# Optimization experiments

Hardware: AMD Instinct MI355X
Metric: run time of the kernel (lower is better)

The kernel has to match this reference:

```python
import jax, jax.numpy as jnp
import numpy as np

DT = 0.03125                                   # ray-march step size
NSTEPS = int(np.ceil(2.0 * np.sqrt(3.0) / DT)) # enough steps to cross the [-1,1]^3 cube diagonal (=111)


def trilinear_sample(vol, pos):
    """vol: [C, D, Hv, Wv]; pos: [H, W, 3] xyz in [-1,1] (grid_sample convention,
    align_corners=True). Returns [C, H, W]."""
    D, Hv, Wv = vol.shape[1], vol.shape[2], vol.shape[3]

    def axis(g, n):
        g = jnp.clip((g + 1.0) * 0.5 * (n - 1), 0.0, n - 1.0)
        i0 = jnp.minimum(jnp.floor(g).astype(jnp.int32), n - 2)
        return i0, i0 + 1, (g - i0)[None]  # frac broadcast over channel dim

    x0, x1, fx = axis(pos[..., 0], Wv)
    y0, y1, fy = axis(pos[..., 1], Hv)
    z0, z1, fz = axis(pos[..., 2], D)

    def g(z, y, x):
        return vol[:, z, y, x]  # [C, H, W]

    c00 = g(z0, y0, x0) * (1 - fx) + g(z0, y0, x1) * fx
    c01 = g(z0, y1, x0) * (1 - fx) + g(z0, y1, x1) * fx
    c10 = g(z1, y0, x0) * (1 - fx) + g(z1, y0, x1) * fx
    c11 = g(z1, y1, x0) * (1 - fx) + g(z1, y1, x1) * fx
    c0 = c00 * (1 - fy) + c01 * fy
    c1 = c10 * (1 - fy) + c11 * fy
    return c0 * (1 - fz) + c1 * fz


def setup_inputs() -> dict:
    key = jax.random.key(0)
    B, H, W, D = 2, 256, 256, 128
    camrot = jnp.tile(jnp.eye(3, dtype=jnp.float32)[None], (B, 1, 1))
    campos = jnp.tile(jnp.array([[0.0, 0.0, -2.5]], dtype=jnp.float32), (B, 1))
    focal = jnp.full((B, 2), 300.0, dtype=jnp.float32)
    princpt = jnp.full((B, 2), 128.0, dtype=jnp.float32)
    ys, xs = jnp.meshgrid(jnp.arange(H, dtype=jnp.float32),
                          jnp.arange(W, dtype=jnp.float32), indexing='ij')
    pixelcoords = jnp.tile(jnp.stack([xs, ys], axis=-1)[None], (B, 1, 1, 1))
    volume = jax.random.uniform(key, (B, 4, D, D, D), dtype=jnp.float32)
    return dict(camrot=camrot, campos=campos, focal=focal, princpt=princpt,
                pixelcoords=pixelcoords, volume=volume)


def reference(camrot, campos, focal, princpt, pixelcoords, volume):
    # camera rays: pixel -> camera -> world (camrot^T applied, as in torch sum over dim=-2)
    raydir = (pixelcoords - princpt[:, None, None, :]) / focal[:, None, None, :]
    raydir = jnp.concatenate([raydir, jnp.ones_like(raydir[..., :1])], axis=-1)
    raydir = jnp.einsum('bij,bhwi->bhwj', camrot, raydir)
    raydir = raydir / jnp.sqrt(jnp.sum(raydir ** 2, axis=-1, keepdims=True))

    # ray-AABB intersection with [-1,1]^3 (no grad, as in torch.no_grad())
    t1 = (-1.0 - campos[:, None, None, :]) / raydir
    t2 = (1.0 - campos[:, None, None, :]) / raydir
    tmin = jnp.maximum(jnp.minimum(t1[..., 0], t2[..., 0]),
                       jnp.maximum(jnp.minimum(t1[..., 1], t2[..., 1]),
                                   jnp.minimum(t1[..., 2], t2[..., 2])))
    tmax = jnp.minimum(jnp.maximum(t1[..., 0], t2[..., 0]),
                       jnp.minimum(jnp.maximum(t1[..., 1], t2[..., 1]),
                                   jnp.maximum(t1[..., 2], t2[..., 2])))
    hit = tmin < tmax
    t0 = jax.lax.stop_gradient(jnp.maximum(jnp.where(hit, tmin, 0.0), 0.0))

    raypos = campos[:, None, None, :] + raydir * t0[..., None]  # [B,H,W,3]
    B, H, W = raypos.shape[:3]
    rayrgb = jnp.zeros((B, 3, H, W), raypos.dtype)
    rayalpha = jnp.zeros((B, 1, H, W), raypos.dtype)

    def step(carry, _):
        raypos, rayrgb, rayalpha = carry
        valid = jnp.all((raypos > -1.0) & (raypos < 1.0), axis=-1).astype(raypos.dtype)
        samp = jax.vmap(trilinear_sample)(volume, raypos)  # [B,4,H,W]
        contrib = (jnp.minimum(rayalpha + samp[:, 3:4] * DT, 1.0) - rayalpha) * valid[:, None]
        rayrgb = rayrgb + samp[:, :3] * contrib
        rayalpha = rayalpha + contrib
        raypos = raypos + raydir * DT
        return (raypos, rayrgb, rayalpha), None

    (_, rayrgb, rayalpha), _ = jax.lax.scan(step, (raypos, rayrgb, rayalpha),
                                            None, length=NSTEPS)
    return jnp.concatenate([rayrgb, rayalpha], axis=1)  # [B,4,H,W]
```

## Files before the change

kernel.cpp:

```cpp
#include <hip/hip_runtime.h>
#include <math.h>

#pragma clang fp contract(off)

#define DT 0.03125f
#define NSTEPS 111

__device__ __forceinline__ float4 lerp4(float4 a, float4 b, float w) {
#pragma clang fp contract(off)
    float wa = 1.0f - w;
    float4 r;
    r.x = a.x * wa + b.x * w;
    r.y = a.y * wa + b.y * w;
    r.z = a.z * wa + b.z * w;
    r.w = a.w * wa + b.w * w;
    return r;
}

__global__ __launch_bounds__(256) void repack_kernel(const float* __restrict__ vol,
                                                     float4* __restrict__ out,
                                                     long total, long spatial) {
    long idx = (long)blockIdx.x * blockDim.x + threadIdx.x;
    if (idx >= total) return;
    long b = idx / spatial;
    long s = idx - b * spatial;
    const float* p = vol + b * 4 * spatial + s;
    float4 v;
    v.x = p[0];
    v.y = p[spatial];
    v.z = p[2 * spatial];
    v.w = p[3 * spatial];
    out[idx] = v;
}

template <bool PACKED>
__global__ __launch_bounds__(256) void raymarch_kernel(
        const float* __restrict__ camrot, const float* __restrict__ campos,
        const float* __restrict__ focal, const float* __restrict__ princpt,
        const float* __restrict__ pixelcoords, const float* __restrict__ vol,
        float* __restrict__ out, int B, int H, int W, int D) {
#pragma clang fp contract(off)
    int x = blockIdx.x * blockDim.x + threadIdx.x;
    int y = blockIdx.y * blockDim.y + threadIdx.y;
    int b = blockIdx.z;
    if (x >= W || y >= H) return;

    long pidx = (((long)b * H + y) * W + x) * 2;
    float px = pixelcoords[pidx];
    float py = pixelcoords[pidx + 1];
    const float* R = camrot + b * 9;
    float cpx = campos[b * 3 + 0], cpy = campos[b * 3 + 1], cpz = campos[b * 3 + 2];
    float flx = focal[b * 2 + 0], fly = focal[b * 2 + 1];
    float prx = princpt[b * 2 + 0], pry = princpt[b * 2 + 1];

    float rx = (px - prx) / flx;
    float ry = (py - pry) / fly;
    float rz = 1.0f;
    float dx = R[0] * rx + R[3] * ry + R[6] * rz;
    float dy = R[1] * rx + R[4] * ry + R[7] * rz;
    float dz = R[2] * rx + R[5] * ry + R[8] * rz;
    float ss = dx * dx;
    ss = ss + dy * dy;
    ss = ss + dz * dz;
    float nrm = sqrtf(ss);
    dx = dx / nrm; dy = dy / nrm; dz = dz / nrm;

    float t1x = (-1.0f - cpx) / dx, t2x = (1.0f - cpx) / dx;
    float t1y = (-1.0f - cpy) / dy, t2y = (1.0f - cpy) / dy;
    float t1z = (-1.0f - cpz) / dz, t2z = (1.0f - cpz) / dz;
    float tmin = fmaxf(fminf(t1x, t2x), fmaxf(fminf(t1y, t2y), fminf(t1z, t2z)));
    float tmax = fminf(fmaxf(t1x, t2x), fminf(fmaxf(t1y, t2y), fmaxf(t1z, t2z)));
    bool hit = tmin < tmax;
    float t0 = fmaxf(hit ? tmin : 0.0f, 0.0f);

    float posx = cpx + dx * t0;
    float posy = cpy + dy * t0;
    float posz = cpz + dz * t0;
    float stx = dx * DT, sty = dy * DT, stz = dz * DT;

    float accr = 0.0f, accg = 0.0f, accb = 0.0f, alpha = 0.0f;
    float gmax = (float)(D - 1);
    long spatial = (long)D * D * D;
    long zstride = (long)D * D;
    const float4* v4 = reinterpret_cast<const float4*>(vol);
    const float* vb = vol + (long)b * 4 * spatial;
    long b4base = (long)b * spatial;

    bool entered = false;
    for (int s = 0; s < NSTEPS; ++s) {
        bool valid = (posx > -1.0f) && (posx < 1.0f) &&
                     (posy > -1.0f) && (posy < 1.0f) &&
                     (posz > -1.0f) && (posz < 1.0f);
        if (valid) {
            entered = true;
            float gx = fminf(fmaxf((posx + 1.0f) * 0.5f * gmax, 0.0f), gmax);
            float gy = fminf(fmaxf((posy + 1.0f) * 0.5f * gmax, 0.0f), gmax);
            float gz = fminf(fmaxf((posz + 1.0f) * 0.5f * gmax, 0.0f), gmax);
            int ix0 = (int)floorf(gx); if (ix0 > D - 2) ix0 = D - 2;
            int iy0 = (int)floorf(gy); if (iy0 > D - 2) iy0 = D - 2;
            int iz0 = (int)floorf(gz); if (iz0 > D - 2) iz0 = D - 2;
            float fx = gx - (float)ix0;
            float fy = gy - (float)iy0;
            float fz = gz - (float)iz0;

            float4 c000, c001, c010, c011, c100, c101, c110, c111;
            if (PACKED) {
                long base = b4base + (long)iz0 * zstride + (long)iy0 * D + ix0;
                c000 = v4[base];
                c001 = v4[base + 1];
                c010 = v4[base + D];
                c011 = v4[base + D + 1];
                c100 = v4[base + zstride];
                c101 = v4[base + zstride + 1];
                c110 = v4[base + zstride + D];
                c111 = v4[base + zstride + D + 1];
            } else {
                long s000 = (long)iz0 * zstride + (long)iy0 * D + ix0;
                #define FETCH(dst, off) { long o_ = (off); \
                    dst.x = vb[o_]; dst.y = vb[o_ + spatial]; \
                    dst.z = vb[o_ + 2 * spatial]; dst.w = vb[o_ + 3 * spatial]; }
                FETCH(c000, s000);
                FETCH(c001, s000 + 1);
                FETCH(c010, s000 + D);
                FETCH(c011, s000 + D + 1);
                FETCH(c100, s000 + zstride);
                FETCH(c101, s000 + zstride + 1);
                FETCH(c110, s000 + zstride + D);
                FETCH(c111, s000 + zstride + D + 1);
                #undef FETCH
            }
            float4 c00 = lerp4(c000, c001, fx);
            float4 c01 = lerp4(c010, c011, fx);
            float4 c10 = lerp4(c100, c101, fx);
            float4 c11 = lerp4(c110, c111, fx);
            float4 c0 = lerp4(c00, c01, fy);
            float4 c1 = lerp4(c10, c11, fy);
            float4 samp = lerp4(c0, c1, fz);

            float contrib = fminf(alpha + samp.w * DT, 1.0f) - alpha;
            accr = accr + samp.x * contrib;
            accg = accg + samp.y * contrib;
            accb = accb + samp.z * contrib;
            alpha = alpha + contrib;
            if (alpha >= 1.0f) break;
        } else if (entered) {
            break;
        }
        posx = posx + stx; posy = posy + sty; posz = posz + stz;
    }

    long hw = (long)H * W;
    long o = (long)b * 4 * hw + (long)y * W + x;
    out[o] = accr;
    out[o + hw] = accg;
    out[o + 2 * hw] = accb;
    out[o + 3 * hw] = alpha;
}

extern "C" void kernel_launch(void* const* d_in, const int* in_sizes, int n_in,
                              void* d_out, int out_size, void* d_ws, size_t ws_size,
                              hipStream_t stream) {
    const float* camrot = (const float*)d_in[0];
    const float* campos = (const float*)d_in[1];
    const float* focal = (const float*)d_in[2];
    const float* princpt = (const float*)d_in[3];
    const float* pixelcoords = (const float*)d_in[4];
    const float* volume = (const float*)d_in[5];
    float* out = (float*)d_out;

    int B = in_sizes[0] / 9;
    long spatial = (long)in_sizes[5] / (B * 4);
    int D = (int)lround(cbrt((double)spatial));
    while ((long)D * D * D > spatial) D--;
    while ((long)(D + 1) * (D + 1) * (D + 1) <= spatial) D++;
    long hw = (long)in_sizes[4] / (B * 2);
    int H = (int)lround(sqrt((double)hw));
    int W = H;

    size_t need = (size_t)B * spatial * 4 * sizeof(float);
    dim3 blk(16, 16, 1);
    dim3 grd((W + 15) / 16, (H + 15) / 16, B);

    if (ws_size >= need) {
        long total = (long)B * spatial;
        int th = 256;
        long nb = (total + th - 1) / th;
        repack_kernel<<<dim3((unsigned)nb), dim3(th), 0, stream>>>(volume, (float4*)d_ws,
                                                                   total, spatial);
        raymarch_kernel<true><<<grd, blk, 0, stream>>>(camrot, campos, focal, princpt,
                                                       pixelcoords, (const float*)d_ws,
                                                       out, B, H, W, D);
    } else {
        raymarch_kernel<false><<<grd, blk, 0, stream>>>(camrot, campos, focal, princpt,
                                                        pixelcoords, volume,
                                                        out, B, H, W, D);
    }
}
```

Baseline: 164.8 us.

## Software-pipeline voxel gathers in raymarch and vectorize volume repack

Replaces the raymarch loop with a two-stage software pipeline. A pre-pass first counts the valid in-cube steps and finds the entry point, then the loads for the next sample are issued while the current one is blended. The early termination on alpha saturation is removed. The repack kernel is vectorized to read float4 quads from each channel and transpose them into interleaved RGBA. This targets gather latency and repack bandwidth, at the cost of higher register use and an extra ALU pre-pass.

```diff
diff --git a/kernel.cpp b/kernel.cpp
--- a/kernel.cpp
+++ b/kernel.cpp
@@ -15,6 +15,26 @@
     r.z = a.z * wa + b.z * w;
     r.w = a.w * wa + b.w * w;
     return r;
+}
+
+
+__global__ __launch_bounds__(256) void repack4_kernel(const float* __restrict__ vol,
+                                                      float4* __restrict__ out,
+                                                      long spatial) {
+    long q = (long)blockIdx.x * blockDim.x + threadIdx.x;
+    long nq = spatial >> 2;
+    if (q >= nq) return;
+    long b = blockIdx.y;
+    const float* p = vol + b * 4 * spatial + (q << 2);
+    float4 c0 = *(const float4*)(p);
+    float4 c1 = *(const float4*)(p + spatial);
+    float4 c2 = *(const float4*)(p + 2 * spatial);
+    float4 c3 = *(const float4*)(p + 3 * spatial);
+    float4* o = out + b * spatial + (q << 2);
+    o[0] = make_float4(c0.x, c1.x, c2.x, c3.x);
+    o[1] = make_float4(c0.y, c1.y, c2.y, c3.y);
+    o[2] = make_float4(c0.z, c1.z, c2.z, c3.z);
+    o[3] = make_float4(c0.w, c1.w, c2.w, c3.w);
 }
 
 __global__ __launch_bounds__(256) void repack_kernel(const float* __restrict__ vol,
@@ -33,11 +53,57 @@
     out[idx] = v;
 }
 
-template <bool PACKED>
-__global__ __launch_bounds__(256) void raymarch_kernel(
+
+__device__ __forceinline__ int voxel_base(float posx, float posy, float posz,
+                                          int D, float gmax, int zstride,
+                                          float& fx, float& fy, float& fz) {
+#pragma clang fp contract(off)
+    float gx = fminf(fmaxf((posx + 1.0f) * 0.5f * gmax, 0.0f), gmax);
+    float gy = fminf(fmaxf((posy + 1.0f) * 0.5f * gmax, 0.0f), gmax);
+    float gz = fminf(fmaxf((posz + 1.0f) * 0.5f * gmax, 0.0f), gmax);
+    int ix0 = (int)floorf(gx); if (ix0 > D - 2) ix0 = D - 2;
+    int iy0 = (int)floorf(gy); if (iy0 > D - 2) iy0 = D - 2;
+    int iz0 = (int)floorf(gz); if (iz0 > D - 2) iz0 = D - 2;
+    fx = gx - (float)ix0;
+    fy = gy - (float)iy0;
+    fz = gz - (float)iz0;
+    return iz0 * zstride + iy0 * D + ix0;
+}
+
+__device__ __forceinline__ void load8(const float4* __restrict__ v4, int base,
+                                      int D, int zstride, float4* c) {
+    c[0] = v4[base];
+    c[1] = v4[base + 1];
+    c[2] = v4[base + D];
+    c[3] = v4[base + D + 1];
+    c[4] = v4[base + zstride];
+    c[5] = v4[base + zstride + 1];
+    c[6] = v4[base + zstride + D];
+    c[7] = v4[base + zstride + D + 1];
+}
+
+__device__ __forceinline__ void accum_step(const float4* c, float fx, float fy, float fz,
+                                           float& accr, float& accg, float& accb,
+                                           float& alpha) {
+#pragma clang fp contract(off)
+    float4 c00 = lerp4(c[0], c[1], fx);
+    float4 c01 = lerp4(c[2], c[3], fx);
+    float4 c10 = lerp4(c[4], c[5], fx);
+    float4 c11 = lerp4(c[6], c[7], fx);
+    float4 c0 = lerp4(c00, c01, fy);
+    float4 c1 = lerp4(c10, c11, fy);
+    float4 samp = lerp4(c0, c1, fz);
+    float contrib = fminf(alpha + samp.w * DT, 1.0f) - alpha;
+    accr = accr + samp.x * contrib;
+    accg = accg + samp.y * contrib;
+    accb = accb + samp.z * contrib;
+    alpha = alpha + contrib;
+}
+
+__global__ __launch_bounds__(256, 1) void raymarch_pipe_kernel(
         const float* __restrict__ camrot, const float* __restrict__ campos,
         const float* __restrict__ focal, const float* __restrict__ princpt,
-        const float* __restrict__ pixelcoords, const float* __restrict__ vol,
+        const float* __restrict__ pixelcoords, const float4* __restrict__ vol4,
         float* __restrict__ out, int B, int H, int W, int D) {
 #pragma clang fp contract(off)
     int x = blockIdx.x * blockDim.x + threadIdx.x;
@@ -78,13 +144,119 @@
     float posz = cpz + dz * t0;
     float stx = dx * DT, sty = dy * DT, stz = dz * DT;
 
+    int n = 0;
+    float e0x = 0.0f, e0y = 0.0f, e0z = 0.0f;
+    {
+        float sx = posx, sy = posy, sz = posz;
+        int firstv = -1;
+        for (int s = 0; s < NSTEPS; ++s) {
+            bool valid = (sx > -1.0f) && (sx < 1.0f) &&
+                         (sy > -1.0f) && (sy < 1.0f) &&
+                         (sz > -1.0f) && (sz < 1.0f);
+            if (valid) {
+                if (firstv < 0) { firstv = s; e0x = sx; e0y = sy; e0z = sz; }
+                n++;
+            } else if (firstv >= 0) {
+                break;
+            }
+            sx = sx + stx; sy = sy + sty; sz = sz + stz;
+        }
+    }
+
+    float accr = 0.0f, accg = 0.0f, accb = 0.0f, alpha = 0.0f;
+    float gmax = (float)(D - 1);
+    int zstride = D * D;
+    int spatial = zstride * D;
+    const float4* v4b = vol4 + (long)b * spatial;
+
+    if (n > 0) {
+        float pxx = e0x, pyy = e0y, pzz = e0z;
+        float fxA, fyA, fzA, fxB = 0.f, fyB = 0.f, fzB = 0.f;
+        float4 A[8], Bv[8];
+
+        int baseA = voxel_base(pxx, pyy, pzz, D, gmax, zstride, fxA, fyA, fzA);
+        load8(v4b, baseA, D, zstride, A);
+        pxx = pxx + stx; pyy = pyy + sty; pzz = pzz + stz;
+
+        if (n > 1) {
+            int baseB = voxel_base(pxx, pyy, pzz, D, gmax, zstride, fxB, fyB, fzB);
+            load8(v4b, baseB, D, zstride, Bv);
+            pxx = pxx + stx; pyy = pyy + sty; pzz = pzz + stz;
+        }
+
+        int i = 0;
+        for (; i + 2 < n; i += 2) {
+            accum_step(A, fxA, fyA, fzA, accr, accg, accb, alpha);
+            int baseA2 = voxel_base(pxx, pyy, pzz, D, gmax, zstride, fxA, fyA, fzA);
+            load8(v4b, baseA2, D, zstride, A);
+            pxx = pxx + stx; pyy = pyy + sty; pzz = pzz + stz;
+
+            accum_step(Bv, fxB, fyB, fzB, accr, accg, accb, alpha);
+            int baseB2 = voxel_base(pxx, pyy, pzz, D, gmax, zstride, fxB, fyB, fzB);
+            load8(v4b, baseB2, D, zstride, Bv);
+            pxx = pxx + stx; pyy = pyy + sty; pzz = pzz + stz;
+        }
+        if (i < n) { accum_step(A, fxA, fyA, fzA, accr, accg, accb, alpha); i++; }
+        if (i < n) { accum_step(Bv, fxB, fyB, fzB, accr, accg, accb, alpha); }
+    }
+
+    long hw = (long)H * W;
+    long o = (long)b * 4 * hw + (long)y * W + x;
+    out[o] = accr;
+    out[o + hw] = accg;
+    out[o + 2 * hw] = accb;
+    out[o + 3 * hw] = alpha;
+}
+
+__global__ __launch_bounds__(256) void raymarch_simple_kernel(
+        const float* __restrict__ camrot, const float* __restrict__ campos,
+        const float* __restrict__ focal, const float* __restrict__ princpt,
+        const float* __restrict__ pixelcoords, const float* __restrict__ vol,
+        float* __restrict__ out, int B, int H, int W, int D) {
+#pragma clang fp contract(off)
+    int x = blockIdx.x * blockDim.x + threadIdx.x;
+    int y = blockIdx.y * blockDim.y + threadIdx.y;
+    int b = blockIdx.z;
+    if (x >= W || y >= H) return;
+
+    long pidx = (((long)b * H + y) * W + x) * 2;
+    float px = pixelcoords[pidx];
+    float py = pixelcoords[pidx + 1];
+    const float* R = camrot + b * 9;
+    float cpx = campos[b * 3 + 0], cpy = campos[b * 3 + 1], cpz = campos[b * 3 + 2];
+    float flx = focal[b * 2 + 0], fly = focal[b * 2 + 1];
+    float prx = princpt[b * 2 + 0], pry = princpt[b * 2 + 1];
+
+    float rx = (px - prx) / flx;
+    float ry = (py - pry) / fly;
+    float rz = 1.0f;
+    float dx = R[0] * rx + R[3] * ry + R[6] * rz;
+    float dy = R[1] * rx + R[4] * ry + R[7] * rz;
+    float dz = R[2] * rx + R[5] * ry + R[8] * rz;
+    float ss = dx * dx;
+    ss = ss + dy * dy;
+    ss = ss + dz * dz;
+    float nrm = sqrtf(ss);
+    dx = dx / nrm; dy = dy / nrm; dz = dz / nrm;
+
+    float t1x = (-1.0f - cpx) / dx, t2x = (1.0f - cpx) / dx;
+    float t1y = (-1.0f - cpy) / dy, t2y = (1.0f - cpy) / dy;
+    float t1z = (-1.0f - cpz) / dz, t2z = (1.0f - cpz) / dz;
+    float tmin = fmaxf(fminf(t1x, t2x), fmaxf(fminf(t1y, t2y), fminf(t1z, t2z)));
+    float tmax = fminf(fmaxf(t1x, t2x), fminf(fmaxf(t1y, t2y), fmaxf(t1z, t2z)));
+    bool hit = tmin < tmax;
+    float t0 = fmaxf(hit ? tmin : 0.0f, 0.0f);
+
+    float posx = cpx + dx * t0;
+    float posy = cpy + dy * t0;
+    float posz = cpz + dz * t0;
+    float stx = dx * DT, sty = dy * DT, stz = dz * DT;
+
     float accr = 0.0f, accg = 0.0f, accb = 0.0f, alpha = 0.0f;
     float gmax = (float)(D - 1);
     long spatial = (long)D * D * D;
     long zstride = (long)D * D;
-    const float4* v4 = reinterpret_cast<const float4*>(vol);
     const float* vb = vol + (long)b * 4 * spatial;
-    long b4base = (long)b * spatial;
 
     bool entered = false;
     for (int s = 0; s < NSTEPS; ++s) {
@@ -103,32 +275,20 @@
             float fy = gy - (float)iy0;
             float fz = gz - (float)iz0;
 
+            long s000 = (long)iz0 * zstride + (long)iy0 * D + ix0;
             float4 c000, c001, c010, c011, c100, c101, c110, c111;
-            if (PACKED) {
-                long base = b4base + (long)iz0 * zstride + (long)iy0 * D + ix0;
-                c000 = v4[base];
-                c001 = v4[base + 1];
-                c010 = v4[base + D];
-                c011 = v4[base + D + 1];
-                c100 = v4[base + zstride];
-                c101 = v4[base + zstride + 1];
-                c110 = v4[base + zstride + D];
-                c111 = v4[base + zstride + D + 1];
-            } else {
-                long s000 = (long)iz0 * zstride + (long)iy0 * D + ix0;
-                #define FETCH(dst, off) { long o_ = (off); \
-                    dst.x = vb[o_]; dst.y = vb[o_ + spatial]; \
-                    dst.z = vb[o_ + 2 * spatial]; dst.w = vb[o_ + 3 * spatial]; }
-                FETCH(c000, s000);
-                FETCH(c001, s000 + 1);
-                FETCH(c010, s000 + D);
-                FETCH(c011, s000 + D + 1);
-                FETCH(c100, s000 + zstride);
-                FETCH(c101, s000 + zstride + 1);
-                FETCH(c110, s000 + zstride + D);
-                FETCH(c111, s000 + zstride + D + 1);
-                #undef FETCH
-            }
+            #define FETCH(dst, off) { long o_ = (off); \
+                dst.x = vb[o_]; dst.y = vb[o_ + spatial]; \
+                dst.z = vb[o_ + 2 * spatial]; dst.w = vb[o_ + 3 * spatial]; }
+            FETCH(c000, s000);
+            FETCH(c001, s000 + 1);
+            FETCH(c010, s000 + D);
+            FETCH(c011, s000 + D + 1);
+            FETCH(c100, s000 + zstride);
+            FETCH(c101, s000 + zstride + 1);
+            FETCH(c110, s000 + zstride + D);
+            FETCH(c111, s000 + zstride + D + 1);
+            #undef FETCH
             float4 c00 = lerp4(c000, c001, fx);
             float4 c01 = lerp4(c010, c011, fx);
             float4 c10 = lerp4(c100, c101, fx);
@@ -182,16 +342,20 @@
     dim3 grd((W + 15) / 16, (H + 15) / 16, B);
 
     if (ws_size >= need) {
-        long total = (long)B * spatial;
-        int th = 256;
-        long nb = (total + th - 1) / th;
-        repack_kernel<<<dim3((unsigned)nb), dim3(th), 0, stream>>>(volume, (float4*)d_ws,
-                                                                   total, spatial);
-        raymarch_kernel<true><<<grd, blk, 0, stream>>>(camrot, campos, focal, princpt,
-                                                       pixelcoords, (const float*)d_ws,
-                                                       out, B, H, W, D);
+        if ((spatial & 3) == 0) {
+            long nq = spatial >> 2;
+            dim3 rgrd((unsigned)((nq + 255) / 256), B, 1);
+            repack4_kernel<<<rgrd, dim3(256), 0, stream>>>(volume, (float4*)d_ws, spatial);
+        } else {
+            long total = (long)B * spatial;
+            repack_kernel<<<dim3((unsigned)((total + 255) / 256)), dim3(256), 0, stream>>>(
+                volume, (float4*)d_ws, total, spatial);
+        }
+        raymarch_pipe_kernel<<<grd, blk, 0, stream>>>(camrot, campos, focal, princpt,
+                                                      pixelcoords, (const float4*)d_ws,
+                                                      out, B, H, W, D);
     } else {
-        raymarch_kernel<false><<<grd, blk, 0, stream>>>(camrot, campos, focal, princpt,
+        raymarch_simple_kernel<<<grd, blk, 0, stream>>>(camrot, campos, focal, princpt,
                                                         pixelcoords, volume,
                                                         out, B, H, W, D);
     }
```

Result: no change. 165.1 us (+0.1%).

## Split ray march into segments with sigma prefix pass and combine

Applied to the files above, without the earlier changes.

Each ray is split into four step segments run by separate threads. A first pass sums alpha increments per segment, and a second pass starts each segment from the clamped prefix alpha and accumulates colour. A combine kernel then adds the partial results. This aims to expose more parallelism and shorten each thread's serial loop, at the cost of a second volume traversal, extra launches, workspace traffic and dropping the early exit on saturated alpha. Starting a segment from the clamped prefix sum is only exact while alpha stays below one. The volume repack is also vectorised to float4 loads.

```diff
diff --git a/kernel.cpp b/kernel.cpp
--- a/kernel.cpp
+++ b/kernel.cpp
@@ -4,17 +4,29 @@
 #pragma clang fp contract(off)
 
 #define DT 0.03125f
+#define INV_DT 32.0f
 #define NSTEPS 111
-
-__device__ __forceinline__ float4 lerp4(float4 a, float4 b, float w) {
-#pragma clang fp contract(off)
-    float wa = 1.0f - w;
-    float4 r;
-    r.x = a.x * wa + b.x * w;
-    r.y = a.y * wa + b.y * w;
-    r.z = a.z * wa + b.z * w;
-    r.w = a.w * wa + b.w * w;
-    return r;
+#define SEG 4
+#define SLEN ((NSTEPS + SEG - 1) / SEG)
+
+
+__global__ __launch_bounds__(256) void repack4_kernel(const float* __restrict__ vol,
+                                                      float4* __restrict__ out,
+                                                      long spatial) {
+    long q = (long)blockIdx.x * blockDim.x + threadIdx.x;
+    long nq = spatial >> 2;
+    if (q >= nq) return;
+    long b = blockIdx.y;
+    const float* p = vol + b * 4 * spatial + (q << 2);
+    float4 c0 = *(const float4*)(p);
+    float4 c1 = *(const float4*)(p + spatial);
+    float4 c2 = *(const float4*)(p + 2 * spatial);
+    float4 c3 = *(const float4*)(p + 3 * spatial);
+    float4* o = out + b * spatial + (q << 2);
+    o[0] = make_float4(c0.x, c1.x, c2.x, c3.x);
+    o[1] = make_float4(c0.y, c1.y, c2.y, c3.y);
+    o[2] = make_float4(c0.z, c1.z, c2.z, c3.z);
+    o[3] = make_float4(c0.w, c1.w, c2.w, c3.w);
 }
 
 __global__ __launch_bounds__(256) void repack_kernel(const float* __restrict__ vol,
@@ -33,18 +45,20 @@
     out[idx] = v;
 }
 
-template <bool PACKED>
-__global__ __launch_bounds__(256) void raymarch_kernel(
-        const float* __restrict__ camrot, const float* __restrict__ campos,
-        const float* __restrict__ focal, const float* __restrict__ princpt,
-        const float* __restrict__ pixelcoords, const float* __restrict__ vol,
-        float* __restrict__ out, int B, int H, int W, int D) {
-#pragma clang fp contract(off)
-    int x = blockIdx.x * blockDim.x + threadIdx.x;
-    int y = blockIdx.y * blockDim.y + threadIdx.y;
-    int b = blockIdx.z;
-    if (x >= W || y >= H) return;
-
+
+struct Ray {
+    float posx, posy, posz;
+    float stx, sty, stz;
+    int n;
+};
+
+__device__ __forceinline__ Ray ray_setup(const float* __restrict__ camrot,
+                                         const float* __restrict__ campos,
+                                         const float* __restrict__ focal,
+                                         const float* __restrict__ princpt,
+                                         const float* __restrict__ pixelcoords,
+                                         int b, int y, int x, int H, int W) {
+#pragma clang fp contract(off)
     long pidx = (((long)b * H + y) * W + x) * 2;
     float px = pixelcoords[pidx];
     float py = pixelcoords[pidx + 1];
@@ -73,80 +87,264 @@
     bool hit = tmin < tmax;
     float t0 = fmaxf(hit ? tmin : 0.0f, 0.0f);
 
-    float posx = cpx + dx * t0;
-    float posy = cpy + dy * t0;
-    float posz = cpz + dz * t0;
-    float stx = dx * DT, sty = dy * DT, stz = dz * DT;
+    Ray r;
+    r.posx = cpx + dx * t0;
+    r.posy = cpy + dy * t0;
+    r.posz = cpz + dz * t0;
+    r.stx = dx * DT; r.sty = dy * DT; r.stz = dz * DT;
+
+    float span = (tmax - t0) * INV_DT + 4.0f;
+    span = fminf(span, (float)NSTEPS);
+    r.n = (hit && span > 0.0f) ? (int)span : 0;
+    return r;
+}
+
+__device__ __forceinline__ int voxel_base(float posx, float posy, float posz,
+                                          int D, float gmax, int zstride,
+                                          float& fx, float& fy, float& fz) {
+#pragma clang fp contract(off)
+    float gx = fminf(fmaxf((posx + 1.0f) * 0.5f * gmax, 0.0f), gmax);
+    float gy = fminf(fmaxf((posy + 1.0f) * 0.5f * gmax, 0.0f), gmax);
+    float gz = fminf(fmaxf((posz + 1.0f) * 0.5f * gmax, 0.0f), gmax);
+    int ix0 = (int)floorf(gx); if (ix0 > D - 2) ix0 = D - 2;
+    int iy0 = (int)floorf(gy); if (iy0 > D - 2) iy0 = D - 2;
+    int iz0 = (int)floorf(gz); if (iz0 > D - 2) iz0 = D - 2;
+    fx = gx - (float)ix0;
+    fy = gy - (float)iy0;
+    fz = gz - (float)iz0;
+    return iz0 * zstride + iy0 * D + ix0;
+}
+
+
+__global__ __launch_bounds__(256, 8) void sigma_pass_kernel(
+        const float* __restrict__ camrot, const float* __restrict__ campos,
+        const float* __restrict__ focal, const float* __restrict__ princpt,
+        const float* __restrict__ pixelcoords, const float4* __restrict__ vol4,
+        float* __restrict__ sums, int B, int H, int W, int D, int nrays) {
+#pragma clang fp contract(off)
+    int x = blockIdx.x * 16 + threadIdx.x;
+    int y = blockIdx.y * 16 + threadIdx.y;
+    int bz = blockIdx.z;
+    int b = bz / SEG;
+    int seg = bz - b * SEG;
+    if (x >= W || y >= H) return;
+    int ray = ((b * H + y) * W + x);
+
+    Ray r = ray_setup(camrot, campos, focal, princpt, pixelcoords, b, y, x, H, W);
+
+    int s0 = seg * SLEN;
+    int s1 = s0 + SLEN; if (s1 > NSTEPS) s1 = NSTEPS;
+    int lim = (r.n < s1) ? r.n : s1;
+
+    float S = 0.0f;
+    if (s0 < lim) {
+        float pxx = r.posx, pyy = r.posy, pzz = r.posz;
+        for (int s = 0; s < s0; ++s) {
+            pxx = pxx + r.stx; pyy = pyy + r.sty; pzz = pzz + r.stz;
+        }
+        float gmax = (float)(D - 1);
+        int zstride = D * D;
+        const float* vw = (const float*)(vol4 + (long)b * ((long)zstride * D));
+        for (int s = s0; s < lim; ++s) {
+            bool inside = (pxx > -1.0f) && (pxx < 1.0f) && (pyy > -1.0f) &&
+                          (pyy < 1.0f) && (pzz > -1.0f) && (pzz < 1.0f);
+            float m = inside ? 1.0f : 0.0f;
+            float fx, fy, fz;
+            int base = voxel_base(pxx, pyy, pzz, D, gmax, zstride, fx, fy, fz);
+            const float* p = vw + (long)base * 4 + 3;
+            float w000 = p[0],               w001 = p[4];
+            float w010 = p[4 * D],           w011 = p[4 * D + 4];
+            float w100 = p[4 * zstride],     w101 = p[4 * zstride + 4];
+            float w110 = p[4 * zstride + 4 * D], w111 = p[4 * zstride + 4 * D + 4];
+            float wa = 1.0f - fx;
+            float c00 = w000 * wa + w001 * fx;
+            float c01 = w010 * wa + w011 * fx;
+            float c10 = w100 * wa + w101 * fx;
+            float c11 = w110 * wa + w111 * fx;
+            float wb = 1.0f - fy;
+            float c0 = c00 * wb + c01 * fy;
+            float c1 = c10 * wb + c11 * fy;
+            float sw = c0 * (1.0f - fz) + c1 * fz;
+            S = S + (sw * DT) * m;
+            pxx = pxx + r.stx; pyy = pyy + r.sty; pzz = pzz + r.stz;
+        }
+    }
+    sums[(long)seg * nrays + ray] = S;
+}
+
+
+__global__ __launch_bounds__(256, 8) void march_pass_kernel(
+        const float* __restrict__ camrot, const float* __restrict__ campos,
+        const float* __restrict__ focal, const float* __restrict__ princpt,
+        const float* __restrict__ pixelcoords, const float4* __restrict__ vol4,
+        const float* __restrict__ sums, float* __restrict__ part,
+        int B, int H, int W, int D, int nrays) {
+#pragma clang fp contract(off)
+    int x = blockIdx.x * 16 + threadIdx.x;
+    int y = blockIdx.y * 16 + threadIdx.y;
+    int bz = blockIdx.z;
+    int b = bz / SEG;
+    int seg = bz - b * SEG;
+    if (x >= W || y >= H) return;
+    int ray = ((b * H + y) * W + x);
+
+    Ray r = ray_setup(camrot, campos, focal, princpt, pixelcoords, b, y, x, H, W);
+
+    float P = 0.0f;
+    for (int j = 0; j < seg; ++j) P = P + sums[(long)j * nrays + ray];
+    float alpha = fminf(P, 1.0f);
+
+    int s0 = seg * SLEN;
+    int s1 = s0 + SLEN; if (s1 > NSTEPS) s1 = NSTEPS;
+    int lim = (r.n < s1) ? r.n : s1;
+
+    float accr = 0.0f, accg = 0.0f, accb = 0.0f;
+    if (s0 < lim) {
+        float pxx = r.posx, pyy = r.posy, pzz = r.posz;
+        for (int s = 0; s < s0; ++s) {
+            pxx = pxx + r.stx; pyy = pyy + r.sty; pzz = pzz + r.stz;
+        }
+        float gmax = (float)(D - 1);
+        int zstride = D * D;
+        const float4* v4b = vol4 + (long)b * ((long)zstride * D);
+        for (int s = s0; s < lim; ++s) {
+            bool inside = (pxx > -1.0f) && (pxx < 1.0f) && (pyy > -1.0f) &&
+                          (pyy < 1.0f) && (pzz > -1.0f) && (pzz < 1.0f);
+            float m = inside ? 1.0f : 0.0f;
+            float fx, fy, fz;
+            int base = voxel_base(pxx, pyy, pzz, D, gmax, zstride, fx, fy, fz);
+            float4 c000 = v4b[base];
+            float4 c001 = v4b[base + 1];
+            float4 c010 = v4b[base + D];
+            float4 c011 = v4b[base + D + 1];
+            float4 c100 = v4b[base + zstride];
+            float4 c101 = v4b[base + zstride + 1];
+            float4 c110 = v4b[base + zstride + D];
+            float4 c111 = v4b[base + zstride + D + 1];
+            float wa = 1.0f - fx;
+            float4 c00, c01, c10, c11, c0, c1, samp;
+            c00.x = c000.x * wa + c001.x * fx; c00.y = c000.y * wa + c001.y * fx;
+            c00.z = c000.z * wa + c001.z * fx; c00.w = c000.w * wa + c001.w * fx;
+            c01.x = c010.x * wa + c011.x * fx; c01.y = c010.y * wa + c011.y * fx;
+            c01.z = c010.z * wa + c011.z * fx; c01.w = c010.w * wa + c011.w * fx;
+            c10.x = c100.x * wa + c101.x * fx; c10.y = c100.y * wa + c101.y * fx;
+            c10.z = c100.z * wa + c101.z * fx; c10.w = c100.w * wa + c101.w * fx;
+            c11.x = c110.x * wa + c111.x * fx; c11.y = c110.y * wa + c111.y * fx;
+            c11.z = c110.z * wa + c111.z * fx; c11.w = c110.w * wa + c111.w * fx;
+            float wb = 1.0f - fy;
+            c0.x = c00.x * wb + c01.x * fy; c0.y = c00.y * wb + c01.y * fy;
+            c0.z = c00.z * wb + c01.z * fy; c0.w = c00.w * wb + c01.w * fy;
+            c1.x = c10.x * wb + c11.x * fy; c1.y = c10.y * wb + c11.y * fy;
+            c1.z = c10.z * wb + c11.z * fy; c1.w = c10.w * wb + c11.w * fy;
+            float wc = 1.0f - fz;
+            samp.x = c0.x * wc + c1.x * fz; samp.y = c0.y * wc + c1.y * fz;
+            samp.z = c0.z * wc + c1.z * fz; samp.w = c0.w * wc + c1.w * fz;
+
+            float contrib = (fminf(alpha + samp.w * DT, 1.0f) - alpha) * m;
+            accr = accr + samp.x * contrib;
+            accg = accg + samp.y * contrib;
+            accb = accb + samp.z * contrib;
+            alpha = alpha + contrib;
+            pxx = pxx + r.stx; pyy = pyy + r.sty; pzz = pzz + r.stz;
+        }
+    }
+    long o = (long)seg * 4 * nrays + ray;
+    part[o] = accr;
+    part[o + nrays] = accg;
+    part[o + 2 * nrays] = accb;
+    part[o + 3 * nrays] = alpha;
+}
+
+
+__global__ __launch_bounds__(256) void combine_kernel(const float* __restrict__ part,
+                                                      float* __restrict__ out,
+                                                      int nrays, int chw) {
+#pragma clang fp contract(off)
+    int ray = blockIdx.x * 256 + threadIdx.x;
+    if (ray >= nrays) return;
+    float r = 0.0f, g = 0.0f, bl = 0.0f;
+    for (int sgi = 0; sgi < SEG; ++sgi) {
+        long o = (long)sgi * 4 * nrays + ray;
+        r = r + part[o];
+        g = g + part[o + nrays];
+        bl = bl + part[o + 2 * nrays];
+    }
+    float a = part[(long)(SEG - 1) * 4 * nrays + 3 * (long)nrays + ray];
+    int b = ray / chw;
+    int pix = ray - b * chw;
+    long o = (long)b * 4 * chw + pix;
+    out[o] = r;
+    out[o + chw] = g;
+    out[o + 2 * chw] = bl;
+    out[o + 3 * chw] = a;
+}
+
+
+__global__ __launch_bounds__(256) void raymarch_simple_kernel(
+        const float* __restrict__ camrot, const float* __restrict__ campos,
+        const float* __restrict__ focal, const float* __restrict__ princpt,
+        const float* __restrict__ pixelcoords, const float* __restrict__ vol,
+        float* __restrict__ out, int B, int H, int W, int D) {
+#pragma clang fp contract(off)
+    int x = blockIdx.x * blockDim.x + threadIdx.x;
+    int y = blockIdx.y * blockDim.y + threadIdx.y;
+    int b = blockIdx.z;
+    if (x >= W || y >= H) return;
+
+    Ray r = ray_setup(camrot, campos, focal, princpt, pixelcoords, b, y, x, H, W);
 
     float accr = 0.0f, accg = 0.0f, accb = 0.0f, alpha = 0.0f;
     float gmax = (float)(D - 1);
     long spatial = (long)D * D * D;
     long zstride = (long)D * D;
-    const float4* v4 = reinterpret_cast<const float4*>(vol);
     const float* vb = vol + (long)b * 4 * spatial;
-    long b4base = (long)b * spatial;
-
-    bool entered = false;
-    for (int s = 0; s < NSTEPS; ++s) {
-        bool valid = (posx > -1.0f) && (posx < 1.0f) &&
-                     (posy > -1.0f) && (posy < 1.0f) &&
-                     (posz > -1.0f) && (posz < 1.0f);
-        if (valid) {
-            entered = true;
-            float gx = fminf(fmaxf((posx + 1.0f) * 0.5f * gmax, 0.0f), gmax);
-            float gy = fminf(fmaxf((posy + 1.0f) * 0.5f * gmax, 0.0f), gmax);
-            float gz = fminf(fmaxf((posz + 1.0f) * 0.5f * gmax, 0.0f), gmax);
-            int ix0 = (int)floorf(gx); if (ix0 > D - 2) ix0 = D - 2;
-            int iy0 = (int)floorf(gy); if (iy0 > D - 2) iy0 = D - 2;
-            int iz0 = (int)floorf(gz); if (iz0 > D - 2) iz0 = D - 2;
-            float fx = gx - (float)ix0;
-            float fy = gy - (float)iy0;
-            float fz = gz - (float)iz0;
-
-            float4 c000, c001, c010, c011, c100, c101, c110, c111;
-            if (PACKED) {
-                long base = b4base + (long)iz0 * zstride + (long)iy0 * D + ix0;
-                c000 = v4[base];
-                c001 = v4[base + 1];
-                c010 = v4[base + D];
-                c011 = v4[base + D + 1];
-                c100 = v4[base + zstride];
-                c101 = v4[base + zstride + 1];
-                c110 = v4[base + zstride + D];
-                c111 = v4[base + zstride + D + 1];
-            } else {
-                long s000 = (long)iz0 * zstride + (long)iy0 * D + ix0;
-                #define FETCH(dst, off) { long o_ = (off); \
-                    dst.x = vb[o_]; dst.y = vb[o_ + spatial]; \
-                    dst.z = vb[o_ + 2 * spatial]; dst.w = vb[o_ + 3 * spatial]; }
-                FETCH(c000, s000);
-                FETCH(c001, s000 + 1);
-                FETCH(c010, s000 + D);
-                FETCH(c011, s000 + D + 1);
-                FETCH(c100, s000 + zstride);
-                FETCH(c101, s000 + zstride + 1);
-                FETCH(c110, s000 + zstride + D);
-                FETCH(c111, s000 + zstride + D + 1);
-                #undef FETCH
-            }
-            float4 c00 = lerp4(c000, c001, fx);
-            float4 c01 = lerp4(c010, c011, fx);
-            float4 c10 = lerp4(c100, c101, fx);
-            float4 c11 = lerp4(c110, c111, fx);
-            float4 c0 = lerp4(c00, c01, fy);
-            float4 c1 = lerp4(c10, c11, fy);
-            float4 samp = lerp4(c0, c1, fz);
-
-            float contrib = fminf(alpha + samp.w * DT, 1.0f) - alpha;
-            accr = accr + samp.x * contrib;
-            accg = accg + samp.y * contrib;
-            accb = accb + samp.z * contrib;
-            alpha = alpha + contrib;
-            if (alpha >= 1.0f) break;
-        } else if (entered) {
-            break;
-        }
-        posx = posx + stx; posy = posy + sty; posz = posz + stz;
+    float pxx = r.posx, pyy = r.posy, pzz = r.posz;
+
+    for (int s = 0; s < r.n; ++s) {
+        bool inside = (pxx > -1.0f) && (pxx < 1.0f) && (pyy > -1.0f) &&
+                      (pyy < 1.0f) && (pzz > -1.0f) && (pzz < 1.0f);
+        float m = inside ? 1.0f : 0.0f;
+        float fx, fy, fz;
+        int base = voxel_base(pxx, pyy, pzz, D, gmax, (int)zstride, fx, fy, fz);
+        long s000 = base;
+        float4 c000, c001, c010, c011, c100, c101, c110, c111;
+        #define FETCH(dst, off) { long o_ = (off); \
+            dst.x = vb[o_]; dst.y = vb[o_ + spatial]; \
+            dst.z = vb[o_ + 2 * spatial]; dst.w = vb[o_ + 3 * spatial]; }
+        FETCH(c000, s000);
+        FETCH(c001, s000 + 1);
+        FETCH(c010, s000 + D);
+        FETCH(c011, s000 + D + 1);
+        FETCH(c100, s000 + zstride);
+        FETCH(c101, s000 + zstride + 1);
+        FETCH(c110, s000 + zstride + D);
+        FETCH(c111, s000 + zstride + D + 1);
+        #undef FETCH
+        float wa = 1.0f - fx;
+        float4 c00, c01, c10, c11, c0, c1, samp;
+        c00.x = c000.x * wa + c001.x * fx; c00.y = c000.y * wa + c001.y * fx;
+        c00.z = c000.z * wa + c001.z * fx; c00.w = c000.w * wa + c001.w * fx;
+        c01.x = c010.x * wa + c011.x * fx; c01.y = c010.y * wa + c011.y * fx;
+        c01.z = c010.z * wa + c011.z * fx; c01.w = c010.w * wa + c011.w * fx;
+        c10.x = c100.x * wa + c101.x * fx; c10.y = c100.y * wa + c101.y * fx;
+        c10.z = c100.z * wa + c101.z * fx; c10.w = c100.w * wa + c101.w * fx;
+        c11.x = c110.x * wa + c111.x * fx; c11.y = c110.y * wa + c111.y * fx;
+        c11.z = c110.z * wa + c111.z * fx; c11.w = c110.w * wa + c111.w * fx;
+        float wb = 1.0f - fy;
+        c0.x = c00.x * wb + c01.x * fy; c0.y = c00.y * wb + c01.y * fy;
+        c0.z = c00.z * wb + c01.z * fy; c0.w = c00.w * wb + c01.w * fy;
+        c1.x = c10.x * wb + c11.x * fy; c1.y = c10.y * wb + c11.y * fy;
+        c1.z = c10.z * wb + c11.z * fy; c1.w = c10.w * wb + c11.w * fy;
+        float wc = 1.0f - fz;
+        samp.x = c0.x * wc + c1.x * fz; samp.y = c0.y * wc + c1.y * fz;
+        samp.z = c0.z * wc + c1.z * fz; samp.w = c0.w * wc + c1.w * fz;
+
+        float contrib = (fminf(alpha + samp.w * DT, 1.0f) - alpha) * m;
+        accr = accr + samp.x * contrib;
+        accg = accg + samp.y * contrib;
+        accb = accb + samp.z * contrib;
+        alpha = alpha + contrib;
+        pxx = pxx + r.stx; pyy = pyy + r.sty; pzz = pzz + r.stz;
     }
 
     long hw = (long)H * W;
@@ -176,22 +374,45 @@
     long hw = (long)in_sizes[4] / (B * 2);
     int H = (int)lround(sqrt((double)hw));
     int W = H;
-
-    size_t need = (size_t)B * spatial * 4 * sizeof(float);
-    dim3 blk(16, 16, 1);
-    dim3 grd((W + 15) / 16, (H + 15) / 16, B);
+    int nrays = (int)(B * hw);
+    int chw = (int)hw;
+
+    size_t vol_bytes = (size_t)B * spatial * 4 * sizeof(float);
+    size_t sums_bytes = (size_t)SEG * nrays * sizeof(float);
+    size_t part_bytes = (size_t)SEG * 4 * nrays * sizeof(float);
+    size_t off_sums = (vol_bytes + 255) & ~(size_t)255;
+    size_t off_part = (off_sums + sums_bytes + 255) & ~(size_t)255;
+    size_t need = off_part + part_bytes;
 
     if (ws_size >= need) {
-        long total = (long)B * spatial;
-        int th = 256;
-        long nb = (total + th - 1) / th;
-        repack_kernel<<<dim3((unsigned)nb), dim3(th), 0, stream>>>(volume, (float4*)d_ws,
-                                                                   total, spatial);
-        raymarch_kernel<true><<<grd, blk, 0, stream>>>(camrot, campos, focal, princpt,
-                                                       pixelcoords, (const float*)d_ws,
-                                                       out, B, H, W, D);
+        float4* vol4 = (float4*)d_ws;
+        float* sums = (float*)((char*)d_ws + off_sums);
+        float* part = (float*)((char*)d_ws + off_part);
+
+        if ((spatial & 3) == 0) {
+            long nq = spatial >> 2;
+            dim3 rgrd((unsigned)((nq + 255) / 256), B, 1);
+            repack4_kernel<<<rgrd, dim3(256), 0, stream>>>(volume, vol4, spatial);
+        } else {
+            long total = (long)B * spatial;
+            repack_kernel<<<dim3((unsigned)((total + 255) / 256)), dim3(256), 0, stream>>>(
+                volume, vol4, total, spatial);
+        }
+
+        dim3 blk(16, 16, 1);
+        dim3 grd((W + 15) / 16, (H + 15) / 16, B * SEG);
+        sigma_pass_kernel<<<grd, blk, 0, stream>>>(camrot, campos, focal, princpt,
+                                                   pixelcoords, vol4, sums,
+                                                   B, H, W, D, nrays);
+        march_pass_kernel<<<grd, blk, 0, stream>>>(camrot, campos, focal, princpt,
+                                                   pixelcoords, vol4, sums, part,
+                                                   B, H, W, D, nrays);
+        combine_kernel<<<dim3((nrays + 255) / 256), dim3(256), 0, stream>>>(
+            part, out, nrays, chw);
     } else {
-        raymarch_kernel<false><<<grd, blk, 0, stream>>>(camrot, campos, focal, princpt,
+        dim3 blk(16, 16, 1);
+        dim3 grd((W + 15) / 16, (H + 15) / 16, B);
+        raymarch_simple_kernel<<<grd, blk, 0, stream>>>(camrot, campos, focal, princpt,
                                                         pixelcoords, volume,
                                                         out, B, H, W, D);
     }
```

Measured after the change: 210.0 us. 27.4% more time.

## Pack volume as fp16 x-neighbor pairs and software-pipeline ray-march gathers

Applied to the files above, without the earlier changes.

The volume is repacked into fp16, and each voxel stores itself together with its +x neighbor for all four channels in one 16-byte uint4. The trilinear sample then needs 4 loads instead of 8 float4 loads, which halves gather traffic and footprint. The march loop now runs a fixed per-ray step count from the slab exit distance, without per-step branching or early exit, and is double-buffered so the next step's loads are issued before the current step is consumed. It also adds a D=128 template specialization and 16x4 blocks, at the cost of fp16 quantization error against the fp32 reference and of removing the alpha-saturation early break.

```diff
diff --git a/kernel.cpp b/kernel.cpp
--- a/kernel.cpp
+++ b/kernel.cpp
@@ -1,9 +1,11 @@
 #include <hip/hip_runtime.h>
+#include <hip/hip_fp16.h>
 #include <math.h>
 
 #pragma clang fp contract(off)
 
 #define DT 0.03125f
+#define INV_DT 32.0f
 #define NSTEPS 111
 
 __device__ __forceinline__ float4 lerp4(float4 a, float4 b, float w) {
@@ -17,34 +19,98 @@
     return r;
 }
 
-__global__ __launch_bounds__(256) void repack_kernel(const float* __restrict__ vol,
-                                                     float4* __restrict__ out,
-                                                     long total, long spatial) {
+
+__device__ __forceinline__ unsigned pack2(float a, float b) {
+    __half2 h = __floats2half2_rn(a, b);
+    return *reinterpret_cast<unsigned*>(&h);
+}
+
+__device__ __forceinline__ void unpack_pair(uint4 u, float4& a, float4& b) {
+    __half2 h01 = *reinterpret_cast<__half2*>(&u.x);
+    __half2 h23 = *reinterpret_cast<__half2*>(&u.y);
+    __half2 h45 = *reinterpret_cast<__half2*>(&u.z);
+    __half2 h67 = *reinterpret_cast<__half2*>(&u.w);
+    float2 f01 = __half22float2(h01);
+    float2 f23 = __half22float2(h23);
+    float2 f45 = __half22float2(h45);
+    float2 f67 = __half22float2(h67);
+    a = make_float4(f01.x, f01.y, f23.x, f23.y);
+    b = make_float4(f45.x, f45.y, f67.x, f67.y);
+}
+
+__global__ __launch_bounds__(256) void repack_pair4_kernel(const float* __restrict__ vol,
+                                                           uint4* __restrict__ out,
+                                                           long spatial, int D) {
+    long chunk = (long)blockIdx.x * blockDim.x + threadIdx.x;
+    long nchunks = spatial >> 2;
+    if (chunk >= nchunks) return;
+    long b = blockIdx.y;
+    long s = chunk << 2;
+    int x0 = (int)(s % D);
+    const float* p = vol + b * 4 * spatial;
+
+    float4 v0 = *(const float4*)(p + s);
+    float4 v1 = *(const float4*)(p + spatial + s);
+    float4 v2 = *(const float4*)(p + 2 * spatial + s);
+    float4 v3 = *(const float4*)(p + 3 * spatial + s);
+    bool last = (x0 + 4 >= D);
+    long sn = last ? (s + 3) : (s + 4);
+    float n0 = p[sn];
+    float n1 = p[spatial + sn];
+    float n2 = p[2 * spatial + sn];
+    float n3 = p[3 * spatial + sn];
+
+    float a0[5] = {v0.x, v0.y, v0.z, v0.w, n0};
+    float a1[5] = {v1.x, v1.y, v1.z, v1.w, n1};
+    float a2[5] = {v2.x, v2.y, v2.z, v2.w, n2};
+    float a3[5] = {v3.x, v3.y, v3.z, v3.w, n3};
+
+    uint4* o = out + b * spatial + s;
+    #pragma unroll
+    for (int k = 0; k < 4; ++k) {
+        uint4 e;
+        e.x = pack2(a0[k], a1[k]);
+        e.y = pack2(a2[k], a3[k]);
+        e.z = pack2(a0[k + 1], a1[k + 1]);
+        e.w = pack2(a2[k + 1], a3[k + 1]);
+        o[k] = e;
+    }
+}
+
+__global__ __launch_bounds__(256) void repack_pair_kernel(const float* __restrict__ vol,
+                                                          uint4* __restrict__ out,
+                                                          long total, long spatial, int D) {
     long idx = (long)blockIdx.x * blockDim.x + threadIdx.x;
     if (idx >= total) return;
     long b = idx / spatial;
     long s = idx - b * spatial;
-    const float* p = vol + b * 4 * spatial + s;
-    float4 v;
-    v.x = p[0];
-    v.y = p[spatial];
-    v.z = p[2 * spatial];
-    v.w = p[3 * spatial];
-    out[idx] = v;
-}
-
-template <bool PACKED>
-__global__ __launch_bounds__(256) void raymarch_kernel(
-        const float* __restrict__ camrot, const float* __restrict__ campos,
-        const float* __restrict__ focal, const float* __restrict__ princpt,
-        const float* __restrict__ pixelcoords, const float* __restrict__ vol,
-        float* __restrict__ out, int B, int H, int W, int D) {
-#pragma clang fp contract(off)
-    int x = blockIdx.x * blockDim.x + threadIdx.x;
-    int y = blockIdx.y * blockDim.y + threadIdx.y;
-    int b = blockIdx.z;
-    if (x >= W || y >= H) return;
-
+    int x = (int)(s % D);
+    long sn = (x < D - 1) ? s + 1 : s;
+    const float* p = vol + b * 4 * spatial;
+    float A0 = p[s], A1 = p[s + spatial], A2 = p[s + 2 * spatial], A3 = p[s + 3 * spatial];
+    float B0 = p[sn], B1 = p[sn + spatial], B2 = p[sn + 2 * spatial], B3 = p[sn + 3 * spatial];
+    uint4 e;
+    e.x = pack2(A0, A1);
+    e.y = pack2(A2, A3);
+    e.z = pack2(B0, B1);
+    e.w = pack2(B2, B3);
+    out[idx] = e;
+}
+
+
+struct Ray {
+    float posx, posy, posz;
+    float stx, sty, stz;
+    int n;
+};
+
+__device__ __forceinline__ Ray ray_setup(const float* __restrict__ camrot,
+                                         const float* __restrict__ campos,
+                                         const float* __restrict__ focal,
+                                         const float* __restrict__ princpt,
+                                         const float* __restrict__ pixelcoords,
+                                         int b, int y, int x, int H, int W) {
+#pragma clang fp contract(off)
     long pidx = (((long)b * H + y) * W + x) * 2;
     float px = pixelcoords[pidx];
     float py = pixelcoords[pidx + 1];
@@ -73,80 +139,164 @@
     bool hit = tmin < tmax;
     float t0 = fmaxf(hit ? tmin : 0.0f, 0.0f);
 
-    float posx = cpx + dx * t0;
-    float posy = cpy + dy * t0;
-    float posz = cpz + dz * t0;
-    float stx = dx * DT, sty = dy * DT, stz = dz * DT;
+    Ray r;
+    r.posx = cpx + dx * t0;
+    r.posy = cpy + dy * t0;
+    r.posz = cpz + dz * t0;
+    r.stx = dx * DT; r.sty = dy * DT; r.stz = dz * DT;
+
+    float span = (tmax - t0) * INV_DT + 4.0f;
+    span = fminf(span, (float)NSTEPS);
+    r.n = (hit && span > 0.0f) ? (int)span : 0;
+    return r;
+}
+
+
+template <int DD>
+__global__ __launch_bounds__(64, 2) void raymarch_fp16_kernel(
+        const float* __restrict__ camrot, const float* __restrict__ campos,
+        const float* __restrict__ focal, const float* __restrict__ princpt,
+        const float* __restrict__ pixelcoords, const uint4* __restrict__ vol,
+        float* __restrict__ out, int B, int H, int W, int Drt) {
+#pragma clang fp contract(off)
+    const int D = (DD > 0) ? DD : Drt;
+    int x = blockIdx.x * 16 + threadIdx.x;
+    int y = blockIdx.y * 4 + threadIdx.y;
+    int b = blockIdx.z;
+    if (x >= W || y >= H) return;
+
+    Ray r = ray_setup(camrot, campos, focal, princpt, pixelcoords, b, y, x, H, W);
+
+    float accr = 0.0f, accg = 0.0f, accb = 0.0f, alpha = 0.0f;
+    float gmax = (float)(D - 1);
+    const int zs = D * D;
+    const uint4* vp = vol + (long)b * ((long)zs * D);
+
+    if (r.n > 0) {
+        float pxx = r.posx, pyy = r.posy, pzz = r.posz;
+        float stx = r.stx, sty = r.sty, stz = r.stz;
+        int spf = 0;
+        uint4 SA0, SA1, SA2, SA3, SB0, SB1, SB2, SB3;
+        float fAx, fAy, fAz, mA, fBx, fBy, fBz, mB;
+
+#define PREFETCH(U0, U1, U2, U3, FX, FY, FZ, M) do {                            \
+        bool inside = (pxx > -1.0f) && (pxx < 1.0f) && (pyy > -1.0f) &&         \
+                      (pyy < 1.0f) && (pzz > -1.0f) && (pzz < 1.0f);            \
+        M = (inside && (spf < NSTEPS)) ? 1.0f : 0.0f;                           \
+        float gx = fminf(fmaxf((pxx + 1.0f) * 0.5f * gmax, 0.0f), gmax);        \
+        float gy = fminf(fmaxf((pyy + 1.0f) * 0.5f * gmax, 0.0f), gmax);        \
+        float gz = fminf(fmaxf((pzz + 1.0f) * 0.5f * gmax, 0.0f), gmax);        \
+        int ix0 = (int)floorf(gx); if (ix0 > D - 2) ix0 = D - 2;                \
+        int iy0 = (int)floorf(gy); if (iy0 > D - 2) iy0 = D - 2;                \
+        int iz0 = (int)floorf(gz); if (iz0 > D - 2) iz0 = D - 2;                \
+        FX = gx - (float)ix0; FY = gy - (float)iy0; FZ = gz - (float)iz0;       \
+        const uint4* p_ = vp + (iz0 * zs + iy0 * D + ix0);                      \
+        U0 = p_[0]; U1 = p_[D]; U2 = p_[zs]; U3 = p_[zs + D];                   \
+        pxx = pxx + stx; pyy = pyy + sty; pzz = pzz + stz;                      \
+        spf = spf + 1;                                                          \
+    } while (0)
+
+#define CONSUME(U0, U1, U2, U3, FX, FY, FZ, M) do {                             \
+        float4 va_, vb_;                                                        \
+        unpack_pair(U0, va_, vb_); float4 c00 = lerp4(va_, vb_, FX);            \
+        unpack_pair(U1, va_, vb_); float4 c01 = lerp4(va_, vb_, FX);            \
+        unpack_pair(U2, va_, vb_); float4 c10 = lerp4(va_, vb_, FX);            \
+        unpack_pair(U3, va_, vb_); float4 c11 = lerp4(va_, vb_, FX);            \
+        float4 c0 = lerp4(c00, c01, FY);                                        \
+        float4 c1 = lerp4(c10, c11, FY);                                        \
+        float4 samp = lerp4(c0, c1, FZ);                                        \
+        float contrib = (fminf(alpha + samp.w * DT, 1.0f) - alpha) * M;         \
+        accr = accr + samp.x * contrib;                                         \
+        accg = accg + samp.y * contrib;                                         \
+        accb = accb + samp.z * contrib;                                         \
+        alpha = alpha + contrib;                                                \
+    } while (0)
+
+        PREFETCH(SA0, SA1, SA2, SA3, fAx, fAy, fAz, mA);
+        PREFETCH(SB0, SB1, SB2, SB3, fBx, fBy, fBz, mB);
+
+        int iters = (r.n + 1) >> 1;
+        for (int it = 0; it < iters; ++it) {
+            CONSUME(SA0, SA1, SA2, SA3, fAx, fAy, fAz, mA);
+            PREFETCH(SA0, SA1, SA2, SA3, fAx, fAy, fAz, mA);
+            CONSUME(SB0, SB1, SB2, SB3, fBx, fBy, fBz, mB);
+            PREFETCH(SB0, SB1, SB2, SB3, fBx, fBy, fBz, mB);
+        }
+#undef PREFETCH
+#undef CONSUME
+    }
+
+    long hw = (long)H * W;
+    long o = (long)b * 4 * hw + (long)y * W + x;
+    out[o] = accr;
+    out[o + hw] = accg;
+    out[o + 2 * hw] = accb;
+    out[o + 3 * hw] = alpha;
+}
+
+
+__global__ __launch_bounds__(256) void raymarch_simple_kernel(
+        const float* __restrict__ camrot, const float* __restrict__ campos,
+        const float* __restrict__ focal, const float* __restrict__ princpt,
+        const float* __restrict__ pixelcoords, const float* __restrict__ vol,
+        float* __restrict__ out, int B, int H, int W, int D) {
+#pragma clang fp contract(off)
+    int x = blockIdx.x * blockDim.x + threadIdx.x;
+    int y = blockIdx.y * blockDim.y + threadIdx.y;
+    int b = blockIdx.z;
+    if (x >= W || y >= H) return;
+
+    Ray r = ray_setup(camrot, campos, focal, princpt, pixelcoords, b, y, x, H, W);
 
     float accr = 0.0f, accg = 0.0f, accb = 0.0f, alpha = 0.0f;
     float gmax = (float)(D - 1);
     long spatial = (long)D * D * D;
     long zstride = (long)D * D;
-    const float4* v4 = reinterpret_cast<const float4*>(vol);
     const float* vb = vol + (long)b * 4 * spatial;
-    long b4base = (long)b * spatial;
-
-    bool entered = false;
-    for (int s = 0; s < NSTEPS; ++s) {
-        bool valid = (posx > -1.0f) && (posx < 1.0f) &&
-                     (posy > -1.0f) && (posy < 1.0f) &&
-                     (posz > -1.0f) && (posz < 1.0f);
-        if (valid) {
-            entered = true;
-            float gx = fminf(fmaxf((posx + 1.0f) * 0.5f * gmax, 0.0f), gmax);
-            float gy = fminf(fmaxf((posy + 1.0f) * 0.5f * gmax, 0.0f), gmax);
-            float gz = fminf(fmaxf((posz + 1.0f) * 0.5f * gmax, 0.0f), gmax);
-            int ix0 = (int)floorf(gx); if (ix0 > D - 2) ix0 = D - 2;
-            int iy0 = (int)floorf(gy); if (iy0 > D - 2) iy0 = D - 2;
-            int iz0 = (int)floorf(gz); if (iz0 > D - 2) iz0 = D - 2;
-            float fx = gx - (float)ix0;
-            float fy = gy - (float)iy0;
-            float fz = gz - (float)iz0;
-
-            float4 c000, c001, c010, c011, c100, c101, c110, c111;
-            if (PACKED) {
-                long base = b4base + (long)iz0 * zstride + (long)iy0 * D + ix0;
-                c000 = v4[base];
-                c001 = v4[base + 1];
-                c010 = v4[base + D];
-                c011 = v4[base + D + 1];
-                c100 = v4[base + zstride];
-                c101 = v4[base + zstride + 1];
-                c110 = v4[base + zstride + D];
-                c111 = v4[base + zstride + D + 1];
-            } else {
-                long s000 = (long)iz0 * zstride + (long)iy0 * D + ix0;
-                #define FETCH(dst, off) { long o_ = (off); \
-                    dst.x = vb[o_]; dst.y = vb[o_ + spatial]; \
-                    dst.z = vb[o_ + 2 * spatial]; dst.w = vb[o_ + 3 * spatial]; }
-                FETCH(c000, s000);
-                FETCH(c001, s000 + 1);
-                FETCH(c010, s000 + D);
-                FETCH(c011, s000 + D + 1);
-                FETCH(c100, s000 + zstride);
-                FETCH(c101, s000 + zstride + 1);
-                FETCH(c110, s000 + zstride + D);
-                FETCH(c111, s000 + zstride + D + 1);
-                #undef FETCH
-            }
-            float4 c00 = lerp4(c000, c001, fx);
-            float4 c01 = lerp4(c010, c011, fx);
-            float4 c10 = lerp4(c100, c101, fx);
-            float4 c11 = lerp4(c110, c111, fx);
-            float4 c0 = lerp4(c00, c01, fy);
-            float4 c1 = lerp4(c10, c11, fy);
-            float4 samp = lerp4(c0, c1, fz);
-
-            float contrib = fminf(alpha + samp.w * DT, 1.0f) - alpha;
-            accr = accr + samp.x * contrib;
-            accg = accg + samp.y * contrib;
-            accb = accb + samp.z * contrib;
-            alpha = alpha + contrib;
-            if (alpha >= 1.0f) break;
-        } else if (entered) {
-            break;
-        }
-        posx = posx + stx; posy = posy + sty; posz = posz + stz;
+    float pxx = r.posx, pyy = r.posy, pzz = r.posz;
+
+    for (int s = 0; s < r.n; ++s) {
+        bool inside = (pxx > -1.0f) && (pxx < 1.0f) && (pyy > -1.0f) &&
+                      (pyy < 1.0f) && (pzz > -1.0f) && (pzz < 1.0f);
+        float m = inside ? 1.0f : 0.0f;
+        float gx = fminf(fmaxf((pxx + 1.0f) * 0.5f * gmax, 0.0f), gmax);
+        float gy = fminf(fmaxf((pyy + 1.0f) * 0.5f * gmax, 0.0f), gmax);
+        float gz = fminf(fmaxf((pzz + 1.0f) * 0.5f * gmax, 0.0f), gmax);
+        int ix0 = (int)floorf(gx); if (ix0 > D - 2) ix0 = D - 2;
+        int iy0 = (int)floorf(gy); if (iy0 > D - 2) iy0 = D - 2;
+        int iz0 = (int)floorf(gz); if (iz0 > D - 2) iz0 = D - 2;
+        float fx = gx - (float)ix0;
+        float fy = gy - (float)iy0;
+        float fz = gz - (float)iz0;
+
+        long s000 = (long)iz0 * zstride + (long)iy0 * D + ix0;
+        float4 c000, c001, c010, c011, c100, c101, c110, c111;
+        #define FETCH(dst, off) { long o_ = (off); \
+            dst.x = vb[o_]; dst.y = vb[o_ + spatial]; \
+            dst.z = vb[o_ + 2 * spatial]; dst.w = vb[o_ + 3 * spatial]; }
+        FETCH(c000, s000);
+        FETCH(c001, s000 + 1);
+        FETCH(c010, s000 + D);
+        FETCH(c011, s000 + D + 1);
+        FETCH(c100, s000 + zstride);
+        FETCH(c101, s000 + zstride + 1);
+        FETCH(c110, s000 + zstride + D);
+        FETCH(c111, s000 + zstride + D + 1);
+        #undef FETCH
+        float4 c00 = lerp4(c000, c001, fx);
+        float4 c01 = lerp4(c010, c011, fx);
+        float4 c10 = lerp4(c100, c101, fx);
+        float4 c11 = lerp4(c110, c111, fx);
+        float4 c0 = lerp4(c00, c01, fy);
+        float4 c1 = lerp4(c10, c11, fy);
+        float4 samp = lerp4(c0, c1, fz);
+
+        float contrib = (fminf(alpha + samp.w * DT, 1.0f) - alpha) * m;
+        accr = accr + samp.x * contrib;
+        accg = accg + samp.y * contrib;
+        accb = accb + samp.z * contrib;
+        alpha = alpha + contrib;
+        pxx = pxx + r.stx; pyy = pyy + r.sty; pzz = pzz + r.stz;
     }
 
     long hw = (long)H * W;
@@ -177,21 +327,32 @@
     int H = (int)lround(sqrt((double)hw));
     int W = H;
 
-    size_t need = (size_t)B * spatial * 4 * sizeof(float);
-    dim3 blk(16, 16, 1);
-    dim3 grd((W + 15) / 16, (H + 15) / 16, B);
-
-    if (ws_size >= need) {
-        long total = (long)B * spatial;
-        int th = 256;
-        long nb = (total + th - 1) / th;
-        repack_kernel<<<dim3((unsigned)nb), dim3(th), 0, stream>>>(volume, (float4*)d_ws,
-                                                                   total, spatial);
-        raymarch_kernel<true><<<grd, blk, 0, stream>>>(camrot, campos, focal, princpt,
-                                                       pixelcoords, (const float*)d_ws,
-                                                       out, B, H, W, D);
+    size_t need = (size_t)B * spatial * sizeof(uint4);
+
+    if (ws_size >= need && D >= 2) {
+        uint4* vol16 = (uint4*)d_ws;
+        if ((D & 3) == 0) {
+            long nchunks = spatial >> 2;
+            dim3 rgrd((unsigned)((nchunks + 255) / 256), B, 1);
+            repack_pair4_kernel<<<rgrd, dim3(256), 0, stream>>>(volume, vol16, spatial, D);
+        } else {
+            long total = (long)B * spatial;
+            repack_pair_kernel<<<dim3((unsigned)((total + 255) / 256)), dim3(256), 0,
+                                 stream>>>(volume, vol16, total, spatial, D);
+        }
+        dim3 blk(16, 4, 1);
+        dim3 grd((W + 15) / 16, (H + 3) / 4, B);
+        if (D == 128) {
+            raymarch_fp16_kernel<128><<<grd, blk, 0, stream>>>(
+                camrot, campos, focal, princpt, pixelcoords, vol16, out, B, H, W, D);
+        } else {
+            raymarch_fp16_kernel<0><<<grd, blk, 0, stream>>>(
+                camrot, campos, focal, princpt, pixelcoords, vol16, out, B, H, W, D);
+        }
     } else {
-        raymarch_kernel<false><<<grd, blk, 0, stream>>>(camrot, campos, focal, princpt,
+        dim3 blk(16, 16, 1);
+        dim3 grd((W + 15) / 16, (H + 15) / 16, B);
+        raymarch_simple_kernel<<<grd, blk, 0, stream>>>(camrot, campos, focal, princpt,
                                                         pixelcoords, volume,
                                                         out, B, H, W, D);
     }
```

New measurement: 175.3 us. 1.06x slower.
